# Kernel tuning notes

Hardware: AMD Instinct MI355X
Metric: run time of the kernel (lower is better)

The kernel has to match this reference:

```python
import jax, jax.numpy as jnp
import numpy as np

N = 10000        # nodes
E = 160000       # edges (no self-loops; conv adds them)
NODE_IN = 64
EDGE_IN = 16
HID = 128        # hidden_dim == out_channels per head
HEADS = 4
LAYERS = 3
NEG = 0.2        # GATv2 leaky_relu negative_slope


def setup_inputs() -> dict:
    key = jax.random.key(0)
    ks = jax.random.split(key, 16)
    x = jax.random.normal(ks[0], (N, NODE_IN), jnp.float32)
    edge_attr = jax.random.normal(ks[1], (E, EDGE_IN), jnp.float32)
    src = jax.random.randint(ks[2], (E,), 0, N, dtype=jnp.int32)
    off = jax.random.randint(ks[3], (E,), 1, N, dtype=jnp.int32)
    dst = (src + off) % N  # guarantees no pre-existing self-loops
    edge_index = jnp.stack([src, dst], axis=0)
    s = 0.05
    params = {
        "node_W": jax.random.normal(ks[4], (NODE_IN, HID), jnp.float32) * s,
        "node_b": jnp.zeros((HID,), jnp.float32),
        "edge_W": jax.random.normal(ks[5], (EDGE_IN, HID), jnp.float32) * s,
        "edge_b": jnp.zeros((HID,), jnp.float32),
        "Wl": jax.random.normal(ks[6], (LAYERS, HID, HEADS * HID), jnp.float32) * s,
        "bl": jnp.zeros((LAYERS, HEADS * HID), jnp.float32),
        "Wr": jax.random.normal(ks[7], (LAYERS, HID, HEADS * HID), jnp.float32) * s,
        "br": jnp.zeros((LAYERS, HEADS * HID), jnp.float32),
        "We": jax.random.normal(ks[8], (LAYERS, HID, HEADS * HID), jnp.float32) * s,  # lin_edge, no bias
        "att": jax.random.normal(ks[9], (LAYERS, HEADS, HID), jnp.float32) * s,
        "bias": jnp.zeros((LAYERS, HID), jnp.float32),  # concat=False final bias
    }
    return {"x": x, "edge_index": edge_index, "edge_attr": edge_attr, **params}


def _gatv2_layer(h, e, src, dst, Wl, bl, Wr, br, We, att, bias):
    # h: [N,HID], e: [E+N,HID] (edge_attr incl. self-loop attrs)
    xl = (h @ Wl + bl).reshape(N, HEADS, HID)   # source transform (lin_l)
    xr = (h @ Wr + br).reshape(N, HEADS, HID)   # target transform (lin_r)
    ee = (e @ We).reshape(-1, HEADS, HID)       # edge transform  (lin_edge)
    m = jax.nn.leaky_relu(xl[src] + xr[dst] + ee, NEG)      # [E',H,C]
    logits = jnp.einsum('ehc,hc->eh', m, att)               # [E',H]
    lmax = jax.ops.segment_max(logits, dst, num_segments=N)  # stable softmax per dst
    p = jnp.exp(logits - lmax[dst])
    denom = jax.ops.segment_sum(p, dst, num_segments=N)
    alpha = p / denom[dst]                                   # [E',H]
    out = jax.ops.segment_sum(alpha[:, :, None] * xl[src], dst, num_segments=N)  # [N,H,C]
    return out.mean(axis=1) + bias  # concat=False -> head mean + bias


def reference(x, edge_index, edge_attr, node_W, node_b, edge_W, edge_b,
              Wl, bl, Wr, br, We, att, bias):
    src, dst = edge_index[0], edge_index[1]
    h = x @ node_W + node_b                       # node_emb
    e = edge_attr @ edge_W + edge_b               # edge_emb
    # add_self_loops(fill_value='mean'): self-loop attr = mean of incoming edge attrs
    ones = jnp.ones((E,), h.dtype)
    deg = jax.ops.segment_sum(ones, dst, num_segments=N)
    e_loop = jax.ops.segment_sum(e, dst, num_segments=N) / jnp.maximum(deg, 1.0)[:, None]
    loop = jnp.arange(N, dtype=src.dtype)
    src_f = jnp.concatenate([src, loop])
    dst_f = jnp.concatenate([dst, loop])
    e_f = jnp.concatenate([e, e_loop], axis=0)    # [E+N, HID]
    for l in range(LAYERS):
        h = jax.nn.relu(_gatv2_layer(h, e_f, src_f, dst_f,
                                     Wl[l], bl[l], Wr[l], br[l], We[l], att[l], bias[l]))
    return h
```

## Files before the change

### kernel.cpp

```cpp
#include <hip/hip_runtime.h>
#include <math.h>

#define N_NODES 10000
#define E_EDGES 160000
#define HID     128
#define HOUT    512
#define NEG_S   0.2f

#define RL(v_, l_) __builtin_amdgcn_readlane((v_), (l_))
__device__ __forceinline__ float rlf(float v, int l) {
  return __uint_as_float(RL(__float_as_uint(v), l));
}

__global__ void k_zero(int* __restrict__ deg) {
  int i = blockIdx.x * 256 + threadIdx.x;
  if (i < N_NODES) deg[i] = 0;
}

__global__ void k_deg(const int* __restrict__ dst, int* __restrict__ deg) {
  int e = blockIdx.x * 256 + threadIdx.x;
  if (e >= E_EDGES) return;
  atomicAdd(&deg[dst[e]], 1);
}

__global__ __launch_bounds__(1024) void k_scan(const int* __restrict__ deg, int* __restrict__ row_ptr) {
  __shared__ int buf[1024];
  int carry = 0;
  if (threadIdx.x == 0) row_ptr[0] = 0;
  for (int base = 0; base < N_NODES; base += 1024) {
    int i = base + (int)threadIdx.x;
    int val = (i < N_NODES) ? (deg[i] + 1) : 0;
    buf[threadIdx.x] = val;
    __syncthreads();
    for (int off = 1; off < 1024; off <<= 1) {
      int t = (threadIdx.x >= (unsigned)off) ? buf[threadIdx.x - off] : 0;
      __syncthreads();
      buf[threadIdx.x] += t;
      __syncthreads();
    }
    if (i < N_NODES) row_ptr[i + 1] = carry + buf[threadIdx.x];
    carry += buf[1023];
    __syncthreads();
  }
}

__global__ void k_csr_init(const int* __restrict__ row_ptr, int* __restrict__ cursor,
                           int* __restrict__ csr_eid) {
  int v = blockIdx.x * 256 + threadIdx.x;
  if (v >= N_NODES) return;
  cursor[v] = 1;
  csr_eid[row_ptr[v]] = E_EDGES + v;
}

__global__ void k_csr_scatter(const int* __restrict__ dst, const int* __restrict__ row_ptr,
                              int* __restrict__ cursor, int* __restrict__ csr_eid) {
  int e = blockIdx.x * 256 + threadIdx.x;
  if (e >= E_EDGES) return;
  int v = dst[e];
  int pos = row_ptr[v] + atomicAdd(&cursor[v], 1);
  csr_eid[pos] = e;
}

__global__ __launch_bounds__(128) void k_node_emb(const float* __restrict__ x,
                                                  const float* __restrict__ W,
                                                  const float* __restrict__ b,
                                                  float* __restrict__ h) {
  __shared__ float sx[64];
  int n = blockIdx.x;
  int c = threadIdx.x;
  if (c < 64) sx[c] = x[(size_t)n * 64 + c];
  __syncthreads();
  float acc = b[c];
#pragma unroll
  for (int k = 0; k < 64; ++k) acc = fmaf(sx[k], W[k * HID + c], acc);
  h[(size_t)n * HID + c] = acc;
}

__global__ __launch_bounds__(512) void k_prep(const float* __restrict__ edge_W,
                                              const float* __restrict__ edge_b,
                                              const float* __restrict__ We,
                                              float* __restrict__ C_all,
                                              float* __restrict__ d_all) {
  int i = blockIdx.x;
  int l = blockIdx.y;
  int j = threadIdx.x;
  const float* wrow = (i < 16) ? (edge_W + i * HID) : edge_b;
  const float* wel = We + (size_t)l * HID * HOUT;
  float acc = 0.f;
  for (int k = 0; k < HID; ++k) acc = fmaf(wrow[k], wel[(size_t)k * HOUT + j], acc);
  if (i < 16) C_all[(size_t)l * 16 * HOUT + (size_t)i * HOUT + j] = acc;
  else        d_all[(size_t)l * HOUT + j] = acc;
}

__global__ __launch_bounds__(256) void k_gemm_xlr(
    const float* __restrict__ A,
    const float* __restrict__ Wl, const float* __restrict__ bl,
    const float* __restrict__ Wr, const float* __restrict__ br,
    float* __restrict__ xl, float* __restrict__ xr) {
  const float* B = blockIdx.z ? Wr : Wl;
  const float* bias = blockIdx.z ? br : bl;
  float* out = blockIdx.z ? xr : xl;
  __shared__ float As[64][128];
  __shared__ float Bs[64][128];
  const int bm = blockIdx.x << 7;
  const int bn = blockIdx.y << 7;
  const int tid = threadIdx.x;
  const int tm = (tid >> 4) << 3;
  const int tn = (tid & 15) << 3;
  float acc[8][8] = {};
  for (int ks = 0; ks < HID; ks += 64) {
#pragma unroll
    for (int i = 0; i < 8; ++i) {
      int q = tid + (i << 8);
      int r = q >> 4;
      int kk = (q & 15) << 2;
      int grow = bm + r;
      float4 av = (grow < N_NODES) ? *(const float4*)(A + (size_t)grow * HID + ks + kk)
                                   : make_float4(0.f, 0.f, 0.f, 0.f);
      int f = ((kk >> 2) & 7) << 2;
      int rc = r ^ f;
      As[kk + 0][rc] = av.x; As[kk + 1][rc] = av.y;
      As[kk + 2][rc] = av.z; As[kk + 3][rc] = av.w;
    }
#pragma unroll
    for (int i = 0; i < 8; ++i) {
      int q = tid + (i << 8);
      int r = q >> 5;
      int nn = (q & 31) << 2;
      *(float4*)(&Bs[r][nn]) = *(const float4*)(B + (size_t)(ks + r) * HOUT + bn + nn);
    }
    __syncthreads();
#pragma unroll 4
    for (int k = 0; k < 64; ++k) {
      int f = ((k >> 2) & 7) << 2;
      float a[8], b[8];
      *(float4*)(&a[0]) = *(const float4*)(&As[k][tm ^ f]);
      *(float4*)(&a[4]) = *(const float4*)(&As[k][(tm + 4) ^ f]);
      *(float4*)(&b[0]) = *(const float4*)(&Bs[k][tn]);
      *(float4*)(&b[4]) = *(const float4*)(&Bs[k][tn + 4]);
#pragma unroll
      for (int i = 0; i < 8; ++i)
#pragma unroll
        for (int j = 0; j < 8; ++j) acc[i][j] = fmaf(a[i], b[j], acc[i][j]);
    }
    __syncthreads();
  }
  float bv[8];
#pragma unroll
  for (int j = 0; j < 8; ++j) bv[j] = bias[bn + tn + j];
#pragma unroll
  for (int i = 0; i < 8; ++i) {
    int grow = bm + tm + i;
    if (grow < N_NODES) {
      float4 s0, s1;
      s0.x = acc[i][0] + bv[0]; s0.y = acc[i][1] + bv[1];
      s0.z = acc[i][2] + bv[2]; s0.w = acc[i][3] + bv[3];
      s1.x = acc[i][4] + bv[4]; s1.y = acc[i][5] + bv[5];
      s1.z = acc[i][6] + bv[6]; s1.w = acc[i][7] + bv[7];
      *(float4*)(out + (size_t)grow * HOUT + bn + tn) = s0;
      *(float4*)(out + (size_t)grow * HOUT + bn + tn + 4) = s1;
    }
  }
}

__device__ __forceinline__ float edge_logit(
    float4 e0, float4 e1, float4 xa, float4 xb,
    float4 xr0, float4 xr1, float4 av0, float4 av1) {
  float t, p;
  t = e0.x + xa.x + xr0.x; t = fmaxf(t, NEG_S * t); p  = t * av0.x;
  t = e0.y + xa.y + xr0.y; t = fmaxf(t, NEG_S * t); p += t * av0.y;
  t = e0.z + xa.z + xr0.z; t = fmaxf(t, NEG_S * t); p += t * av0.z;
  t = e0.w + xa.w + xr0.w; t = fmaxf(t, NEG_S * t); p += t * av0.w;
  t = e1.x + xb.x + xr1.x; t = fmaxf(t, NEG_S * t); p += t * av1.x;
  t = e1.y + xb.y + xr1.y; t = fmaxf(t, NEG_S * t); p += t * av1.y;
  t = e1.z + xb.z + xr1.z; t = fmaxf(t, NEG_S * t); p += t * av1.z;
  t = e1.w + xb.w + xr1.w; t = fmaxf(t, NEG_S * t); p += t * av1.w;
#pragma unroll
  for (int off = 1; off <= 8; off <<= 1) p += __shfl_xor(p, off);
  return p;
}

#define EEACC(q, c0, c1, A, B) \
  A.x = fmaf(q, c0.x, A.x); A.y = fmaf(q, c0.y, A.y); \
  A.z = fmaf(q, c0.z, A.z); A.w = fmaf(q, c0.w, A.w); \
  B.x = fmaf(q, c1.x, B.x); B.y = fmaf(q, c1.y, B.y); \
  B.z = fmaf(q, c1.z, B.z); B.w = fmaf(q, c1.w, B.w);

__global__ __launch_bounds__(512) void k_fused(
    const float* __restrict__ xl, const float* __restrict__ xr,
    const float* __restrict__ edge_attr, const int* __restrict__ src,
    const int* __restrict__ row_ptr, const int* __restrict__ csr_eid,
    const float* __restrict__ C, const float* __restrict__ dvec,
    const float* __restrict__ att, const float* __restrict__ bias,
    float* __restrict__ hout) {
  __shared__ float Cs[16 * 512];
  const int tid = threadIdx.x;
#pragma unroll
  for (int i = 0; i < 4; ++i)
    *(float4*)(&Cs[i * 2048 + tid * 4]) = *(const float4*)(C + i * 2048 + tid * 4);
  __syncthreads();

  const int wid = tid >> 6, lane = tid & 63;
  const int v = blockIdx.x * 8 + wid;
  if (v >= N_NODES) return;
  const int r0 = row_ptr[v], r1 = row_ptr[v + 1];
  const int cnt = r1 - r0 - 1;
  const int kk = lane & 15, slot = lane >> 4;
  const int cb = lane * 8;

  float4 av0 = *(const float4*)(att + cb),  av1 = *(const float4*)(att + cb + 4);
  float4 dv0 = *(const float4*)(dvec + cb), dv1 = *(const float4*)(dvec + cb + 4);
  float4 xr0 = *(const float4*)(xr + (size_t)v * HOUT + cb);
  float4 xr1 = *(const float4*)(xr + (size_t)v * HOUT + cb + 4);

  float o0=0,o1=0,o2=0,o3=0,o4=0,o5=0,o6=0,o7=0;
  float m = -1e30f, s = 0.f, psum = 0.f;

  for (int g = 0; g < cnt; g += 4) {
    int idx = g + slot;
    bool valL = idx < cnt;
    int pos = r0 + 1 + (valL ? idx : 0);
    int eid = csr_eid[pos];
    int sv  = src[eid];
    float ea = valL ? edge_attr[(size_t)eid * 16 + kk] : 0.f;
    psum += ea;

    int sv0 = RL(sv, 0), sv1 = RL(sv, 16), sv2 = RL(sv, 32), sv3 = RL(sv, 48);
    const float4* xp0 = (const float4*)(xl + (size_t)sv0 * HOUT + cb);
    const float4* xp1 = (const float4*)(xl + (size_t)sv1 * HOUT + cb);
    const float4* xp2 = (const float4*)(xl + (size_t)sv2 * HOUT + cb);
    const float4* xp3 = (const float4*)(xl + (size_t)sv3 * HOUT + cb);
    float4 xa0 = xp0[0], xb0 = xp0[1];
    float4 xa1 = xp1[0], xb1 = xp1[1];
    float4 xa2 = xp2[0], xb2 = xp2[1];
    float4 xa3 = xp3[0], xb3 = xp3[1];

    float4 eA0 = dv0, eB0 = dv1, eA1 = dv0, eB1 = dv1;
    float4 eA2 = dv0, eB2 = dv1, eA3 = dv0, eB3 = dv1;
    unsigned eau = __float_as_uint(ea);
#pragma unroll
    for (int k = 0; k < 16; ++k) {
      float4 c0 = *(const float4*)(&Cs[k * 512 + cb]);
      float4 c1 = *(const float4*)(&Cs[k * 512 + cb + 4]);
      float q0 = __uint_as_float(RL(eau, k));
      float q1 = __uint_as_float(RL(eau, 16 + k));
      float q2 = __uint_as_float(RL(eau, 32 + k));
      float q3 = __uint_as_float(RL(eau, 48 + k));
      EEACC(q0, c0, c1, eA0, eB0)
      EEACC(q1, c0, c1, eA1, eB1)
      EEACC(q2, c0, c1, eA2, eB2)
      EEACC(q3, c0, c1, eA3, eB3)
    }

    float lg0 = edge_logit(eA0, eB0, xa0, xb0, xr0, xr1, av0, av1);
    float lg1 = edge_logit(eA1, eB1, xa1, xb1, xr0, xr1, av0, av1);
    float lg2 = edge_logit(eA2, eB2, xa2, xb2, xr0, xr1, av0, av1);
    float lg3 = edge_logit(eA3, eB3, xa3, xb3, xr0, xr1, av0, av1);
    if (g + 1 >= cnt) lg1 = -1e30f;
    if (g + 2 >= cnt) lg2 = -1e30f;
    if (g + 3 >= cnt) lg3 = -1e30f;

    float gm = fmaxf(fmaxf(lg0, lg1), fmaxf(lg2, lg3));
    float mn = fmaxf(m, gm);
    float sc = __expf(m - mn);
    float p0 = __expf(lg0 - mn), p1 = __expf(lg1 - mn);
    float p2 = __expf(lg2 - mn), p3 = __expf(lg3 - mn);
    m = mn;
    s = s * sc + (p0 + p1) + (p2 + p3);
    o0 = o0*sc + p0*xa0.x + p1*xa1.x + p2*xa2.x + p3*xa3.x;
    o1 = o1*sc + p0*xa0.y + p1*xa1.y + p2*xa2.y + p3*xa3.y;
    o2 = o2*sc + p0*xa0.z + p1*xa1.z + p2*xa2.z + p3*xa3.z;
    o3 = o3*sc + p0*xa0.w + p1*xa1.w + p2*xa2.w + p3*xa3.w;
    o4 = o4*sc + p0*xb0.x + p1*xb1.x + p2*xb2.x + p3*xb3.x;
    o5 = o5*sc + p0*xb0.y + p1*xb1.y + p2*xb2.y + p3*xb3.y;
    o6 = o6*sc + p0*xb0.z + p1*xb1.z + p2*xb2.z + p3*xb3.z;
    o7 = o7*sc + p0*xb0.w + p1*xb1.w + p2*xb2.w + p3*xb3.w;
  }

  psum += __shfl_xor(psum, 16);
  psum += __shfl_xor(psum, 32);
  float invd = (cnt > 0) ? (1.f / (float)cnt) : 0.f;
  float mea = psum * invd;
  float4 sA, sB;
  if (cnt > 0) { sA = dv0; sB = dv1; }
  else { sA = make_float4(0,0,0,0); sB = make_float4(0,0,0,0); }
  unsigned mu = __float_as_uint(mea);
#pragma unroll
  for (int k = 0; k < 16; ++k) {
    float4 c0 = *(const float4*)(&Cs[k * 512 + cb]);
    float4 c1 = *(const float4*)(&Cs[k * 512 + cb + 4]);
    float q = __uint_as_float(RL(mu, k));
    EEACC(q, c0, c1, sA, sB)
  }
  const float4* xsp = (const float4*)(xl + (size_t)v * HOUT + cb);
  float4 xsa = xsp[0], xsb = xsp[1];
  float lgS = edge_logit(sA, sB, xsa, xsb, xr0, xr1, av0, av1);
  {
    float mn = fmaxf(m, lgS);
    float sc = __expf(m - mn);
    float pS = __expf(lgS - mn);
    m = mn;
    s = s * sc + pS;
    o0 = o0*sc + pS*xsa.x; o1 = o1*sc + pS*xsa.y;
    o2 = o2*sc + pS*xsa.z; o3 = o3*sc + pS*xsa.w;
    o4 = o4*sc + pS*xsb.x; o5 = o5*sc + pS*xsb.y;
    o6 = o6*sc + pS*xsb.z; o7 = o7*sc + pS*xsb.w;
  }

  float inv_s = 1.f / s;
  float r[8] = {o0*inv_s, o1*inv_s, o2*inv_s, o3*inv_s,
                o4*inv_s, o5*inv_s, o6*inv_s, o7*inv_s};
#pragma unroll
  for (int j = 0; j < 8; ++j) {
    float t = r[j];
    t += __shfl_xor(t, 16);
    t += __shfl_xor(t, 32);
    r[j] = t * 0.25f;
  }
  if (lane < 16) {
    float4 w0, w1;
    w0.x = fmaxf(r[0] + bias[cb + 0], 0.f); w0.y = fmaxf(r[1] + bias[cb + 1], 0.f);
    w0.z = fmaxf(r[2] + bias[cb + 2], 0.f); w0.w = fmaxf(r[3] + bias[cb + 3], 0.f);
    w1.x = fmaxf(r[4] + bias[cb + 4], 0.f); w1.y = fmaxf(r[5] + bias[cb + 5], 0.f);
    w1.z = fmaxf(r[6] + bias[cb + 6], 0.f); w1.w = fmaxf(r[7] + bias[cb + 7], 0.f);
    *(float4*)(hout + (size_t)v * HID + cb) = w0;
    *(float4*)(hout + (size_t)v * HID + cb + 4) = w1;
  }
}

extern "C" void kernel_launch(void* const* d_in, const int* in_sizes, int n_in,
                              void* d_out, int out_size, void* d_ws, size_t ws_size,
                              hipStream_t stream) {
  const float* x         = (const float*)d_in[0];
  const int*   ei        = (const int*)d_in[1];
  const float* edge_attr = (const float*)d_in[2];
  const float* node_W    = (const float*)d_in[3];
  const float* node_b    = (const float*)d_in[4];
  const float* edge_W    = (const float*)d_in[5];
  const float* edge_b    = (const float*)d_in[6];
  const float* Wl        = (const float*)d_in[7];
  const float* bl        = (const float*)d_in[8];
  const float* Wr        = (const float*)d_in[9];
  const float* br        = (const float*)d_in[10];
  const float* We        = (const float*)d_in[11];
  const float* att       = (const float*)d_in[12];
  const float* bias      = (const float*)d_in[13];
  float* out = (float*)d_out;
  const int* src = ei;
  const int* dst = ei + E_EDGES;

  char* p = (char*)d_ws;
  auto alloc = [&](size_t bytes) { char* r = p; p += (bytes + 255) & ~(size_t)255; return r; };
  float* h_a     = (float*)alloc((size_t)N_NODES * HID * 4);
  float* h_b     = (float*)alloc((size_t)N_NODES * HID * 4);
  float* xl      = (float*)alloc((size_t)N_NODES * HOUT * 4);
  float* xr      = (float*)alloc((size_t)N_NODES * HOUT * 4);
  float* C_all   = (float*)alloc((size_t)3 * 16 * HOUT * 4);
  float* d_all   = (float*)alloc((size_t)3 * HOUT * 4);
  int* deg       = (int*)alloc((size_t)N_NODES * 4);
  int* row_ptr   = (int*)alloc((size_t)(N_NODES + 1) * 4);
  int* cursor    = (int*)alloc((size_t)N_NODES * 4);
  int* csr_eid   = (int*)alloc((size_t)(E_EDGES + N_NODES) * 4);

  k_zero<<<(N_NODES + 255) / 256, 256, 0, stream>>>(deg);
  k_deg<<<(E_EDGES + 255) / 256, 256, 0, stream>>>(dst, deg);
  k_scan<<<1, 1024, 0, stream>>>(deg, row_ptr);
  k_csr_init<<<(N_NODES + 255) / 256, 256, 0, stream>>>(row_ptr, cursor, csr_eid);
  k_csr_scatter<<<(E_EDGES + 255) / 256, 256, 0, stream>>>(dst, row_ptr, cursor, csr_eid);
  k_node_emb<<<N_NODES, 128, 0, stream>>>(x, node_W, node_b, h_a);
  k_prep<<<dim3(17, 3), 512, 0, stream>>>(edge_W, edge_b, We, C_all, d_all);

  for (int l = 0; l < 3; ++l) {
    const float* hin = (l == 0) ? h_a : ((l == 1) ? h_b : h_a);
    float* hout = (l == 0) ? h_b : ((l == 1) ? h_a : out);
    k_gemm_xlr<<<dim3(79, 4, 2), 256, 0, stream>>>(
        hin, Wl + (size_t)l * HID * HOUT, bl + (size_t)l * HOUT,
        Wr + (size_t)l * HID * HOUT, br + (size_t)l * HOUT, xl, xr);
    k_fused<<<(N_NODES + 7) / 8, 512, 0, stream>>>(
        xl, xr, edge_attr, src, row_ptr, csr_eid,
        C_all + (size_t)l * 16 * HOUT, d_all + (size_t)l * HOUT,
        att + (size_t)l * HOUT, bias + (size_t)l * HID, hout);
  }
}
```

Measured before the change: 619.8 us.

## Retile xl/xr GEMM with resident B and prefetch edge indices in fused kernel

Restructures the per-layer xl/xr GEMM so each block keeps a 128x64 slice of the weight matrix resident in shared memory and loops over five 64-row chunks of nodes with 4x4 per-thread tiles, using a 32x8x2 grid. In the fused attention kernel, xr and the edge bias vector are folded into one base vector so the per-edge logit does fewer adds. The next group's csr index, source id and edge attribute are software-prefetched while the current group is computed. The smaller GEMM tile lowers arithmetic intensity per thread, and the prefetch uses extra registers in a 512-thread kernel.

```diff
diff --git a/kernel.cpp b/kernel.cpp
--- a/kernel.cpp
+++ b/kernel.cpp
@@ -8,9 +8,6 @@
 #define NEG_S   0.2f
 
 #define RL(v_, l_) __builtin_amdgcn_readlane((v_), (l_))
-__device__ __forceinline__ float rlf(float v, int l) {
-  return __uint_as_float(RL(__float_as_uint(v), l));
-}
 
 __global__ void k_zero(int* __restrict__ deg) {
   int i = blockIdx.x * 256 + threadIdx.x;
@@ -100,81 +97,80 @@
   const float* B = blockIdx.z ? Wr : Wl;
   const float* bias = blockIdx.z ? br : bl;
   float* out = blockIdx.z ? xr : xl;
-  __shared__ float As[64][128];
-  __shared__ float Bs[64][128];
-  const int bm = blockIdx.x << 7;
-  const int bn = blockIdx.y << 7;
+  __shared__ float Bs[128][64];
+  __shared__ float As[128][64];
   const int tid = threadIdx.x;
-  const int tm = (tid >> 4) << 3;
-  const int tn = (tid & 15) << 3;
-  float acc[8][8] = {};
-  for (int ks = 0; ks < HID; ks += 64) {
+  const int bn = blockIdx.y << 6;
+
+#pragma unroll
+  for (int i = 0; i < 8; ++i) {
+    int linear = tid + (i << 8);
+    int kr = linear >> 4;
+    int cq = (linear & 15) << 2;
+    *(float4*)(&Bs[kr][cq]) = *(const float4*)(B + (size_t)kr * HOUT + bn + cq);
+  }
+
+  const int tr = tid >> 4;
+  const int tc = tid & 15;
+  float4 bv = *(const float4*)(bias + bn + (tc << 2));
+
+  for (int ch = 0; ch < 5; ++ch) {
+    int rbase = blockIdx.x * 320 + (ch << 6);
+    __syncthreads();
 #pragma unroll
     for (int i = 0; i < 8; ++i) {
-      int q = tid + (i << 8);
-      int r = q >> 4;
-      int kk = (q & 15) << 2;
-      int grow = bm + r;
-      float4 av = (grow < N_NODES) ? *(const float4*)(A + (size_t)grow * HID + ks + kk)
+      int linear = tid + (i << 8);
+      int kq = linear & 31;
+      int r  = linear >> 5;
+      int grow = rbase + r;
+      float4 av = (grow < N_NODES) ? *(const float4*)(A + (size_t)grow * HID + (kq << 2))
                                    : make_float4(0.f, 0.f, 0.f, 0.f);
-      int f = ((kk >> 2) & 7) << 2;
-      int rc = r ^ f;
+      int kk = kq << 2;
+      int rc = r ^ ((kq & 7) << 2);
       As[kk + 0][rc] = av.x; As[kk + 1][rc] = av.y;
       As[kk + 2][rc] = av.z; As[kk + 3][rc] = av.w;
     }
-#pragma unroll
-    for (int i = 0; i < 8; ++i) {
-      int q = tid + (i << 8);
-      int r = q >> 5;
-      int nn = (q & 31) << 2;
-      *(float4*)(&Bs[r][nn]) = *(const float4*)(B + (size_t)(ks + r) * HOUT + bn + nn);
-    }
     __syncthreads();
-#pragma unroll 4
-    for (int k = 0; k < 64; ++k) {
+
+    float acc[4][4] = {};
+#pragma unroll 16
+    for (int k = 0; k < HID; ++k) {
       int f = ((k >> 2) & 7) << 2;
-      float a[8], b[8];
-      *(float4*)(&a[0]) = *(const float4*)(&As[k][tm ^ f]);
-      *(float4*)(&a[4]) = *(const float4*)(&As[k][(tm + 4) ^ f]);
-      *(float4*)(&b[0]) = *(const float4*)(&Bs[k][tn]);
-      *(float4*)(&b[4]) = *(const float4*)(&Bs[k][tn + 4]);
-#pragma unroll
-      for (int i = 0; i < 8; ++i)
-#pragma unroll
-        for (int j = 0; j < 8; ++j) acc[i][j] = fmaf(a[i], b[j], acc[i][j]);
-    }
-    __syncthreads();
-  }
-  float bv[8];
-#pragma unroll
-  for (int j = 0; j < 8; ++j) bv[j] = bias[bn + tn + j];
-#pragma unroll
-  for (int i = 0; i < 8; ++i) {
-    int grow = bm + tm + i;
-    if (grow < N_NODES) {
-      float4 s0, s1;
-      s0.x = acc[i][0] + bv[0]; s0.y = acc[i][1] + bv[1];
-      s0.z = acc[i][2] + bv[2]; s0.w = acc[i][3] + bv[3];
-      s1.x = acc[i][4] + bv[4]; s1.y = acc[i][5] + bv[5];
-      s1.z = acc[i][6] + bv[6]; s1.w = acc[i][7] + bv[7];
-      *(float4*)(out + (size_t)grow * HOUT + bn + tn) = s0;
-      *(float4*)(out + (size_t)grow * HOUT + bn + tn + 4) = s1;
+      float4 a = *(const float4*)(&As[k][(tr << 2) ^ f]);
+      float4 b = *(const float4*)(&Bs[k][tc << 2]);
+      acc[0][0] = fmaf(a.x, b.x, acc[0][0]); acc[0][1] = fmaf(a.x, b.y, acc[0][1]);
+      acc[0][2] = fmaf(a.x, b.z, acc[0][2]); acc[0][3] = fmaf(a.x, b.w, acc[0][3]);
+      acc[1][0] = fmaf(a.y, b.x, acc[1][0]); acc[1][1] = fmaf(a.y, b.y, acc[1][1]);
+      acc[1][2] = fmaf(a.y, b.z, acc[1][2]); acc[1][3] = fmaf(a.y, b.w, acc[1][3]);
+      acc[2][0] = fmaf(a.z, b.x, acc[2][0]); acc[2][1] = fmaf(a.z, b.y, acc[2][1]);
+      acc[2][2] = fmaf(a.z, b.z, acc[2][2]); acc[2][3] = fmaf(a.z, b.w, acc[2][3]);
+      acc[3][0] = fmaf(a.w, b.x, acc[3][0]); acc[3][1] = fmaf(a.w, b.y, acc[3][1]);
+      acc[3][2] = fmaf(a.w, b.z, acc[3][2]); acc[3][3] = fmaf(a.w, b.w, acc[3][3]);
+    }
+#pragma unroll
+    for (int i = 0; i < 4; ++i) {
+      int grow = rbase + (tr << 2) + i;
+      if (grow < N_NODES) {
+        float4 sv;
+        sv.x = acc[i][0] + bv.x; sv.y = acc[i][1] + bv.y;
+        sv.z = acc[i][2] + bv.z; sv.w = acc[i][3] + bv.w;
+        *(float4*)(out + (size_t)grow * HOUT + bn + (tc << 2)) = sv;
+      }
     }
   }
 }
 
 __device__ __forceinline__ float edge_logit(
-    float4 e0, float4 e1, float4 xa, float4 xb,
-    float4 xr0, float4 xr1, float4 av0, float4 av1) {
+    float4 e0, float4 e1, float4 xa, float4 xb, float4 av0, float4 av1) {
   float t, p;
-  t = e0.x + xa.x + xr0.x; t = fmaxf(t, NEG_S * t); p  = t * av0.x;
-  t = e0.y + xa.y + xr0.y; t = fmaxf(t, NEG_S * t); p += t * av0.y;
-  t = e0.z + xa.z + xr0.z; t = fmaxf(t, NEG_S * t); p += t * av0.z;
-  t = e0.w + xa.w + xr0.w; t = fmaxf(t, NEG_S * t); p += t * av0.w;
-  t = e1.x + xb.x + xr1.x; t = fmaxf(t, NEG_S * t); p += t * av1.x;
-  t = e1.y + xb.y + xr1.y; t = fmaxf(t, NEG_S * t); p += t * av1.y;
-  t = e1.z + xb.z + xr1.z; t = fmaxf(t, NEG_S * t); p += t * av1.z;
-  t = e1.w + xb.w + xr1.w; t = fmaxf(t, NEG_S * t); p += t * av1.w;
+  t = e0.x + xa.x; t = fmaxf(t, NEG_S * t); p  = t * av0.x;
+  t = e0.y + xa.y; t = fmaxf(t, NEG_S * t); p += t * av0.y;
+  t = e0.z + xa.z; t = fmaxf(t, NEG_S * t); p += t * av0.z;
+  t = e0.w + xa.w; t = fmaxf(t, NEG_S * t); p += t * av0.w;
+  t = e1.x + xb.x; t = fmaxf(t, NEG_S * t); p += t * av1.x;
+  t = e1.y + xb.y; t = fmaxf(t, NEG_S * t); p += t * av1.y;
+  t = e1.z + xb.z; t = fmaxf(t, NEG_S * t); p += t * av1.z;
+  t = e1.w + xb.w; t = fmaxf(t, NEG_S * t); p += t * av1.w;
 #pragma unroll
   for (int off = 1; off <= 8; off <<= 1) p += __shfl_xor(p, off);
   return p;
@@ -209,22 +205,28 @@
   const int cb = lane * 8;
 
   float4 av0 = *(const float4*)(att + cb),  av1 = *(const float4*)(att + cb + 4);
-  float4 dv0 = *(const float4*)(dvec + cb), dv1 = *(const float4*)(dvec + cb + 4);
-  float4 xr0 = *(const float4*)(xr + (size_t)v * HOUT + cb);
-  float4 xr1 = *(const float4*)(xr + (size_t)v * HOUT + cb + 4);
+  float4 base0 = *(const float4*)(xr + (size_t)v * HOUT + cb);
+  float4 base1 = *(const float4*)(xr + (size_t)v * HOUT + cb + 4);
+  if (cnt > 0) {
+    float4 dv0 = *(const float4*)(dvec + cb), dv1 = *(const float4*)(dvec + cb + 4);
+    base0.x += dv0.x; base0.y += dv0.y; base0.z += dv0.z; base0.w += dv0.w;
+    base1.x += dv1.x; base1.y += dv1.y; base1.z += dv1.z; base1.w += dv1.w;
+  }
 
   float o0=0,o1=0,o2=0,o3=0,o4=0,o5=0,o6=0,o7=0;
   float m = -1e30f, s = 0.f, psum = 0.f;
 
-  for (int g = 0; g < cnt; g += 4) {
-    int idx = g + slot;
+  int sv = 0; float ea = 0.f;
+  if (cnt > 0) {
+    int idx = slot;
     bool valL = idx < cnt;
     int pos = r0 + 1 + (valL ? idx : 0);
     int eid = csr_eid[pos];
-    int sv  = src[eid];
-    float ea = valL ? edge_attr[(size_t)eid * 16 + kk] : 0.f;
-    psum += ea;
-
+    sv = src[eid];
+    ea = valL ? edge_attr[(size_t)eid * 16 + kk] : 0.f;
+  }
+
+  for (int g = 0; g < cnt; g += 4) {
     int sv0 = RL(sv, 0), sv1 = RL(sv, 16), sv2 = RL(sv, 32), sv3 = RL(sv, 48);
     const float4* xp0 = (const float4*)(xl + (size_t)sv0 * HOUT + cb);
     const float4* xp1 = (const float4*)(xl + (size_t)sv1 * HOUT + cb);
@@ -234,10 +236,21 @@
     float4 xa1 = xp1[0], xb1 = xp1[1];
     float4 xa2 = xp2[0], xb2 = xp2[1];
     float4 xa3 = xp3[0], xb3 = xp3[1];
-
-    float4 eA0 = dv0, eB0 = dv1, eA1 = dv0, eB1 = dv1;
-    float4 eA2 = dv0, eB2 = dv1, eA3 = dv0, eB3 = dv1;
+    psum += ea;
     unsigned eau = __float_as_uint(ea);
+
+    int nsv = 0; float nea = 0.f;
+    if (g + 4 < cnt) {
+      int idx = g + 4 + slot;
+      bool valL = idx < cnt;
+      int pos = r0 + 1 + (valL ? idx : 0);
+      int eid = csr_eid[pos];
+      nsv = src[eid];
+      nea = valL ? edge_attr[(size_t)eid * 16 + kk] : 0.f;
+    }
+
+    float4 eA0 = base0, eB0 = base1, eA1 = base0, eB1 = base1;
+    float4 eA2 = base0, eB2 = base1, eA3 = base0, eB3 = base1;
 #pragma unroll
     for (int k = 0; k < 16; ++k) {
       float4 c0 = *(const float4*)(&Cs[k * 512 + cb]);
@@ -252,10 +265,10 @@
       EEACC(q3, c0, c1, eA3, eB3)
     }
 
-    float lg0 = edge_logit(eA0, eB0, xa0, xb0, xr0, xr1, av0, av1);
-    float lg1 = edge_logit(eA1, eB1, xa1, xb1, xr0, xr1, av0, av1);
-    float lg2 = edge_logit(eA2, eB2, xa2, xb2, xr0, xr1, av0, av1);
-    float lg3 = edge_logit(eA3, eB3, xa3, xb3, xr0, xr1, av0, av1);
+    float lg0 = edge_logit(eA0, eB0, xa0, xb0, av0, av1);
+    float lg1 = edge_logit(eA1, eB1, xa1, xb1, av0, av1);
+    float lg2 = edge_logit(eA2, eB2, xa2, xb2, av0, av1);
+    float lg3 = edge_logit(eA3, eB3, xa3, xb3, av0, av1);
     if (g + 1 >= cnt) lg1 = -1e30f;
     if (g + 2 >= cnt) lg2 = -1e30f;
     if (g + 3 >= cnt) lg3 = -1e30f;
@@ -275,15 +288,15 @@
     o5 = o5*sc + p0*xb0.y + p1*xb1.y + p2*xb2.y + p3*xb3.y;
     o6 = o6*sc + p0*xb0.z + p1*xb1.z + p2*xb2.z + p3*xb3.z;
     o7 = o7*sc + p0*xb0.w + p1*xb1.w + p2*xb2.w + p3*xb3.w;
+
+    sv = nsv; ea = nea;
   }
 
   psum += __shfl_xor(psum, 16);
   psum += __shfl_xor(psum, 32);
   float invd = (cnt > 0) ? (1.f / (float)cnt) : 0.f;
   float mea = psum * invd;
-  float4 sA, sB;
-  if (cnt > 0) { sA = dv0; sB = dv1; }
-  else { sA = make_float4(0,0,0,0); sB = make_float4(0,0,0,0); }
+  float4 sA = base0, sB = base1;
   unsigned mu = __float_as_uint(mea);
 #pragma unroll
   for (int k = 0; k < 16; ++k) {
@@ -294,7 +307,7 @@
   }
   const float4* xsp = (const float4*)(xl + (size_t)v * HOUT + cb);
   float4 xsa = xsp[0], xsb = xsp[1];
-  float lgS = edge_logit(sA, sB, xsa, xsb, xr0, xr1, av0, av1);
+  float lgS = edge_logit(sA, sB, xsa, xsb, av0, av1);
   {
     float mn = fmaxf(m, lgS);
     float sc = __expf(m - mn);
@@ -373,7 +386,7 @@
   for (int l = 0; l < 3; ++l) {
     const float* hin = (l == 0) ? h_a : ((l == 1) ? h_b : h_a);
     float* hout = (l == 0) ? h_b : ((l == 1) ? h_a : out);
-    k_gemm_xlr<<<dim3(79, 4, 2), 256, 0, stream>>>(
+    k_gemm_xlr<<<dim3(32, 8, 2), 256, 0, stream>>>(
         hin, Wl + (size_t)l * HID * HOUT, bl + (size_t)l * HOUT,
         Wr + (size_t)l * HID * HOUT, br + (size_t)l * HOUT, xl, xr);
     k_fused<<<(N_NODES + 7) / 8, 512, 0, stream>>>(
```

After: 625.6 us. Within noise of the previous version (+0.9%).
